# Kernel optimization log

Measured on AMD Instinct MI355X. Metric: run time of the kernel, lower is better.

## Reference

```python
import jax, jax.numpy as jnp
import numpy as np

B, S, D = 4, 1024, 4096
HQ, HKV, HD = 32, 8, 128
GROUPS = HQ // HKV
SCALE = 1.0 / np.sqrt(HD)


def setup_inputs() -> dict:
    key = jax.random.key(0)
    ks = jax.random.split(key, 7)
    inv_freq = 1.0 / (10000.0 ** (jnp.arange(0, HD, 2, dtype=jnp.float32) / HD))
    pos = jnp.arange(S, dtype=jnp.float32)
    freqs = pos[:, None] * inv_freq[None, :]           # [S, HD/2]
    emb = jnp.concatenate([freqs, freqs], axis=-1)      # [S, HD] (duplicated halves)
    return {
        "hidden_states": jax.random.normal(ks[0], (B, S, D), dtype=jnp.float32) * 0.02,
        "cos": jnp.cos(emb)[None],                       # [1, S, HD]
        "sin": jnp.sin(emb)[None],                       # [1, S, HD]
        "Wq": jax.random.normal(ks[1], (HQ * HD, D), dtype=jnp.float32) * 0.02,
        "Wk": jax.random.normal(ks[2], (HKV * HD, D), dtype=jnp.float32) * 0.02,
        "Wv": jax.random.normal(ks[3], (HKV * HD, D), dtype=jnp.float32) * 0.02,
        "Wo": jax.random.normal(ks[4], (D, HQ * HD), dtype=jnp.float32) * 0.02,
    }


def _rope(x, cos_h, sin_h):
    # x: [B, S, H, HD]; cos_h/sin_h: [S, HD/2] (non-interleaved rotate-half)
    half = x.shape[-1] // 2
    x1, x2 = x[..., :half], x[..., half:]
    c = cos_h[None, :, None, :]
    s = sin_h[None, :, None, :]
    return jnp.concatenate([x1 * c - x2 * s, x2 * c + x1 * s], axis=-1)


def reference(hidden_states, cos, sin, Wq, Wk, Wv, Wo):
    b, s, d = hidden_states.shape
    # projections (torch Linear: y = x @ W.T)
    q = (hidden_states @ Wq.T).reshape(b, s, HQ, HD)
    k = (hidden_states @ Wk.T).reshape(b, s, HKV, HD)
    v = (hidden_states @ Wv.T).reshape(b, s, HKV, HD)
    # module slices the second half of the [1, S, HD] tables
    cos_h = cos[0, :, HD // 2:]
    sin_h = sin[0, :, HD // 2:]
    q = _rope(q, cos_h, sin_h)
    k = _rope(k, cos_h, sin_h)
    # GQA: repeat each kv head GROUPS times (consecutively, as repeat_kv does)
    k = jnp.repeat(k, GROUPS, axis=2)                    # [B, S, HQ, HD]
    v = jnp.repeat(v, GROUPS, axis=2)
    # full (non-causal) SDPA, as in the source (no mask passed)
    scores = jnp.einsum("bqhd,bkhd->bhqk", q, k) * SCALE
    probs = jax.nn.softmax(scores, axis=-1)
    attn = jnp.einsum("bhqk,bkhd->bqhd", probs, v)
    attn = attn.reshape(b, s, HQ * HD)
    return attn @ Wo.T
```

## Files before the change

kernel.cpp:

```cpp
#include <hip/hip_runtime.h>
#include <hip/hip_bf16.h>
#include <stdint.h>


typedef __attribute__((ext_vector_type(8))) short s8_t;
typedef __attribute__((ext_vector_type(4))) float f4_t;
typedef __attribute__((ext_vector_type(4))) unsigned short us4_t;

#define MFMA16(a, b, c) __builtin_amdgcn_mfma_f32_16x16x32_bf16((a), (b), (c), 0, 0, 0)

__device__ __forceinline__ float b2f(unsigned short u) {
  union { unsigned int i; float f; } x; x.i = ((unsigned int)u) << 16; return x.f;
}
__device__ __forceinline__ unsigned short f2b(float f) {
  union { float f; unsigned int i; } x; x.f = f;
  unsigned int r = x.i + 0x7fff + ((x.i >> 16) & 1);
  return (unsigned short)(r >> 16);
}

__device__ __forceinline__ bool probe_is_f32_off(const void* p, int off) {
  if (!p) return false;
  const unsigned short* u = (const unsigned short*)p + off;
  bool f = false;
#pragma unroll
  for (int i = 0; i < 64; ++i) {
    const float v = b2f(u[i]);
    f |= !(fabsf(v) < 1e8f);
  }
  return f;
}
__device__ __forceinline__ bool probe_is_f32(const void* p) {
  return probe_is_f32_off(p, 0);
}

__device__ __forceinline__ s8_t cvt8(const float* p) {
  const float4 a = *(const float4*)(p);
  const float4 b = *(const float4*)(p + 4);
  union { s8_t v; __hip_bfloat162 h[4]; } t;
  t.h[0] = __float22bfloat162_rn(make_float2(a.x, a.y));
  t.h[1] = __float22bfloat162_rn(make_float2(a.z, a.w));
  t.h[2] = __float22bfloat162_rn(make_float2(b.x, b.y));
  t.h[3] = __float22bfloat162_rn(make_float2(b.z, b.w));
  return t.v;
}

__device__ __forceinline__ s8_t load8(const void* base, size_t off, bool f32) {
  if (f32) return cvt8((const float*)base + off);
  return *(const s8_t*)((const unsigned short*)base + off);
}

__global__ __launch_bounds__(256) void cvt_to_bf16(
    unsigned short* __restrict__ out, const void* __restrict__ in)
{
  const bool f = probe_is_f32(in);
  const size_t i = ((size_t)blockIdx.x * 256 + threadIdx.x) * 8;
  if (f) *(s8_t*)(out + i) = cvt8((const float*)in + i);
  else   *(s8_t*)(out + i) = *(const s8_t*)((const unsigned short*)in + i);
}

__global__ __launch_bounds__(256) void gemm_bt(
    void* __restrict__ C,
    const void* __restrict__ A,
    const void* __restrict__ B,
    int M, int N, int K,
    const void* probeA, const void* probeB, const void* probeC,
    int transC)
{
  constexpr int LP = 72;
  __shared__ unsigned short sA[128 * LP];
  __shared__ unsigned short sB[128 * LP];
  const bool fA = probe_is_f32(probeA);
  const bool fB = probe_is_f32(probeB);
  const bool fC = probe_is_f32(probeC);

  const int tid  = threadIdx.x;
  const int lane = tid & 63;
  const int wv   = tid >> 6;
  const int wr   = (wv >> 1) * 64;
  const int wc   = (wv & 1) * 64;
  const int quad = lane >> 4;
  const int l16  = lane & 15;
  const int m0 = blockIdx.x * 128;
  const int n0 = blockIdx.y * 128;

  f4_t acc[4][4];
#pragma unroll
  for (int i = 0; i < 4; ++i)
#pragma unroll
    for (int j = 0; j < 4; ++j) acc[i][j] = (f4_t){0.f, 0.f, 0.f, 0.f};

  int srow[4], scol[4];
#pragma unroll
  for (int it = 0; it < 4; ++it) {
    const int s = it * 256 + tid;
    srow[it] = s >> 3;
    scol[it] = (s & 7) * 8;
  }

  const int nK = K >> 6;
  for (int kt = 0; kt < nK; ++kt) {
    const int k0 = kt << 6;
    s8_t va[4], vb[4];
#pragma unroll
    for (int it = 0; it < 4; ++it) {
      va[it] = load8(A, (size_t)(m0 + srow[it]) * K + k0 + scol[it], fA);
      vb[it] = load8(B, (size_t)(n0 + srow[it]) * K + k0 + scol[it], fB);
    }
#pragma unroll
    for (int it = 0; it < 4; ++it) {
      *(s8_t*)(&sA[srow[it] * LP + scol[it]]) = va[it];
      *(s8_t*)(&sB[srow[it] * LP + scol[it]]) = vb[it];
    }
    __syncthreads();
#pragma unroll
    for (int kc = 0; kc < 2; ++kc) {
      s8_t af[4], bf[4];
#pragma unroll
      for (int i = 0; i < 4; ++i) {
        af[i] = *(const s8_t*)(&sA[(wr + i * 16 + l16) * LP + (kc * 4 + quad) * 8]);
        bf[i] = *(const s8_t*)(&sB[(wc + i * 16 + l16) * LP + (kc * 4 + quad) * 8]);
      }
#pragma unroll
      for (int i = 0; i < 4; ++i)
#pragma unroll
        for (int j = 0; j < 4; ++j)
          acc[i][j] = MFMA16(af[i], bf[j], acc[i][j]);
    }
    __syncthreads();
  }

  if (transC) {
#pragma unroll
    for (int i = 0; i < 4; ++i) {
      const int rbase = m0 + wr + i * 16 + quad * 4;
#pragma unroll
      for (int j = 0; j < 4; ++j) {
        const int col = n0 + wc + j * 16 + l16;
        us4_t t;
#pragma unroll
        for (int rg = 0; rg < 4; ++rg) t[rg] = f2b(acc[i][j][rg]);
        *(us4_t*)(&((unsigned short*)C)[(size_t)col * M + rbase]) = t;
      }
    }
  } else {
#pragma unroll
    for (int i = 0; i < 4; ++i) {
      const int rbase = m0 + wr + i * 16 + quad * 4;
#pragma unroll
      for (int j = 0; j < 4; ++j) {
        const int col = n0 + wc + j * 16 + l16;
#pragma unroll
        for (int rg = 0; rg < 4; ++rg) {
          const size_t idx = (size_t)(rbase + rg) * N + col;
          if (fC) ((float*)C)[idx] = acc[i][j][rg];
          else    ((unsigned short*)C)[idx] = f2b(acc[i][j][rg]);
        }
      }
    }
  }
}

__global__ __launch_bounds__(256) void rope_kernel(
    unsigned short* __restrict__ X,
    const void* __restrict__ cosb,
    const void* __restrict__ sinb,
    int log2nh, int mode)
{
  bool f;
  if (mode == 1)      f = true;
  else if (mode == 2) f = false;
  else f = probe_is_f32_off(cosb, 2048) | probe_is_f32_off(sinb, 2048);
  const size_t idx = (size_t)blockIdx.x * 256 + threadIdx.x;
  const int jb = (int)(idx & 7) * 8;
  const size_t row = idx >> 3;
  const int s = (int)((row >> log2nh) & 1023);
  unsigned short* p = X + row * 128;
  union { s8_t v; unsigned short u[8]; } ua, ub, o1, o2;
  ua.v = *(const s8_t*)(p + jb);
  ub.v = *(const s8_t*)(p + 64 + jb);
#pragma unroll
  for (int j = 0; j < 8; ++j) {
    const int ci = s * 128 + 64 + jb + j;
    const float c  = f ? ((const float*)cosb)[ci] : b2f(((const unsigned short*)cosb)[ci]);
    const float sn = f ? ((const float*)sinb)[ci] : b2f(((const unsigned short*)sinb)[ci]);
    const float x1 = b2f(ua.u[j]);
    const float x2 = b2f(ub.u[j]);
    o1.u[j] = f2b(x1 * c - x2 * sn);
    o2.u[j] = f2b(x2 * c + x1 * sn);
  }
  *(s8_t*)(p + jb)      = o1.v;
  *(s8_t*)(p + 64 + jb) = o2.v;
}

__global__ __launch_bounds__(256) void attn_kernel(
    unsigned short* O,
    const unsigned short* Q,
    const unsigned short* __restrict__ Kb,
    const unsigned short* __restrict__ Vt)
{
  constexpr int S = 1024, HQ = 32, HKV = 8, HD = 128;
  constexpr int SCP = 1048;
  constexpr int QP  = 152;
  constexpr float SCALE = 0.08838834764831845f;
  __shared__ unsigned short sc[16 * SCP];
  __shared__ unsigned short sq[16 * QP];
  __shared__ float s_linv[16];

  const int bid = blockIdx.x;
  const int qt = bid & 63;
  const int h  = (bid >> 6) & 31;
  const int b  = bid >> 11;
  const int kh = h >> 2;
  const int tid  = threadIdx.x;
  const int lane = tid & 63;
  const int wv   = tid >> 6;
  const int quad = lane >> 4;
  const int l16  = lane & 15;

  const unsigned short* Qg = Q  + ((size_t)(b * S + qt * 16) * HQ + h) * HD;
  const unsigned short* Kg = Kb + ((size_t)b * S * HKV + kh) * HD;
  const unsigned short* Vg = Vt + ((size_t)kh * HD) * 4096 + (size_t)b * S;

  {
    const int r = tid >> 4, c = (tid & 15) * 8;
    *(s8_t*)(&sq[r * QP + c]) = *(const s8_t*)(Qg + (size_t)r * (HQ * HD) + c);
  }
  __syncthreads();

#pragma unroll 2
  for (int kt = 0; kt < 16; ++kt) {
    const int ks = wv * 256 + kt * 16;
    f4_t acc = (f4_t){0.f, 0.f, 0.f, 0.f};
#pragma unroll
    for (int kc = 0; kc < 4; ++kc) {
      const s8_t qa = *(const s8_t*)(&sq[l16 * QP + kc * 32 + quad * 8]);
      const s8_t kf = *(const s8_t*)(Kg + (size_t)(ks + l16) * (HKV * HD) + kc * 32 + quad * 8);
      acc = MFMA16(qa, kf, acc);
    }
#pragma unroll
    for (int rg = 0; rg < 4; ++rg)
      sc[(quad * 4 + rg) * SCP + ks + l16] = f2b(acc[rg] * SCALE);
  }
  __syncthreads();

  {
    const int r = tid >> 4, c0 = tid & 15;
    unsigned short* srow = &sc[r * SCP + c0 * 8];
    float mx = -1e30f;
#pragma unroll
    for (int u = 0; u < 8; ++u) {
      union { s8_t v; unsigned short us[8]; } t;
      t.v = *(const s8_t*)(srow + u * 128);
#pragma unroll
      for (int j = 0; j < 8; ++j) mx = fmaxf(mx, b2f(t.us[j]));
    }
#pragma unroll
    for (int off = 8; off; off >>= 1) mx = fmaxf(mx, __shfl_xor(mx, off, 16));
    float sum = 0.f;
#pragma unroll
    for (int u = 0; u < 8; ++u) {
      union { s8_t v; unsigned short us[8]; } t;
      t.v = *(const s8_t*)(srow + u * 128);
#pragma unroll
      for (int j = 0; j < 8; ++j) {
        const float e = __expf(b2f(t.us[j]) - mx);
        sum += e;
        t.us[j] = f2b(e);
      }
      *(s8_t*)(srow + u * 128) = t.v;
    }
#pragma unroll
    for (int off = 8; off; off >>= 1) sum += __shfl_xor(sum, off, 16);
    if (c0 == 0) s_linv[r] = 1.0f / sum;
  }
  __syncthreads();

  f4_t oacc[2];
  oacc[0] = (f4_t){0.f, 0.f, 0.f, 0.f};
  oacc[1] = (f4_t){0.f, 0.f, 0.f, 0.f};
  const unsigned short* vb0 = Vg + (size_t)(wv * 32 + l16) * 4096 + quad * 8;
  const unsigned short* vb1 = vb0 + (size_t)16 * 4096;
  const unsigned short* prow = &sc[l16 * SCP + quad * 8];
#pragma unroll 2
  for (int ck = 0; ck < 16; ++ck) {
#pragma unroll
    for (int kc = 0; kc < 2; ++kc) {
      const int ko = ck * 64 + kc * 32;
      const s8_t pa = *(const s8_t*)(prow + ko);
      const s8_t v0 = *(const s8_t*)(vb0 + ko);
      const s8_t v1 = *(const s8_t*)(vb1 + ko);
      oacc[0] = MFMA16(pa, v0, oacc[0]);
      oacc[1] = MFMA16(pa, v1, oacc[1]);
    }
  }

#pragma unroll
  for (int dt = 0; dt < 2; ++dt)
#pragma unroll
    for (int rg = 0; rg < 4; ++rg) {
      const int r = quad * 4 + rg;
      const int d = wv * 32 + dt * 16 + l16;
      O[((size_t)(b * S + qt * 16 + r) * HQ + h) * HD + d] =
          f2b(oacc[dt][rg] * s_linv[r]);
    }
}

extern "C" void kernel_launch(void* const* d_in, const int* in_sizes, int n_in,
                              void* d_out, int out_size, void* d_ws, size_t ws_size,
                              hipStream_t stream)
{
  const void* hs   = d_in[0];
  const void* cosb = d_in[1];
  const void* sinb = d_in[2];
  const void* Wq   = d_in[3];
  const void* Wk   = d_in[4];
  const void* Wv   = d_in[5];
  const void* Wo   = d_in[6];

  const size_t MB = (size_t)1 << 20;
  const bool f32in = (n_in >= 1 && in_sizes && in_sizes[0] == (int)(64 * MB));
  int rmode = 0;
  if (in_sizes && n_in >= 2) {
    if (in_sizes[1] == 524288) rmode = 1;
    else if (in_sizes[1] == 262144) rmode = 2;
  }

  unsigned short* Qb = (unsigned short*)d_ws;
  unsigned short* Kb = (unsigned short*)d_out;
  unsigned short* Vt = (unsigned short*)d_out + 4194304;

  const void* hsA = hs;
  if (f32in && out_size >= (int)(48 * MB)) {
    unsigned short* hs_b = (unsigned short*)d_out + 8388608;
    cvt_to_bf16<<<8192, 256, 0, stream>>>(hs_b, hs);
    hsA = hs_b;
  }
  const void* WqB = Wq;
  if (f32in && ws_size >= 64 * MB) {
    unsigned short* wq_b = (unsigned short*)d_ws + 16777216;
    cvt_to_bf16<<<8192, 256, 0, stream>>>(wq_b, Wq);
    WqB = wq_b;
  }
  const void* WoB = Wo;
  if (f32in && ws_size >= 96 * MB) {
    unsigned short* wo_b = (unsigned short*)d_ws + 33554432;
    cvt_to_bf16<<<8192, 256, 0, stream>>>(wo_b, Wo);
    WoB = wo_b;
  }

  gemm_bt<<<dim3(32,  8), 256, 0, stream>>>(Kb, hsA, Wk, 4096, 1024, 4096,
                                            hsA, Wk, nullptr, 0);
  gemm_bt<<<dim3(32,  8), 256, 0, stream>>>(Vt, hsA, Wv, 4096, 1024, 4096,
                                            hsA, Wv, nullptr, 1);
  gemm_bt<<<dim3(32, 32), 256, 0, stream>>>(Qb, hsA, WqB, 4096, 4096, 4096,
                                            hsA, WqB, nullptr, 0);
  rope_kernel<<<4096, 256, 0, stream>>>(Qb, cosb, sinb, 5, rmode);
  rope_kernel<<<1024, 256, 0, stream>>>(Kb, cosb, sinb, 3, rmode);
  attn_kernel<<<4 * 32 * 64, 256, 0, stream>>>(Qb, Qb, Kb, Vt);
  gemm_bt<<<dim3(32, 32), 256, 0, stream>>>(d_out, Qb, WoB, 4096, 4096, 4096,
                                            nullptr, WoB, hs, 0);
}
```

Before: 1.939 ms.

## Use direct global-to-LDS loads in GEMM, pre-convert Wk/Wv, tune attention kernel

```diff
diff --git a/kernel.cpp b/kernel.cpp
--- a/kernel.cpp
+++ b/kernel.cpp
@@ -16,6 +16,13 @@
   union { float f; unsigned int i; } x; x.f = f;
   unsigned int r = x.i + 0x7fff + ((x.i >> 16) & 1);
   return (unsigned short)(r >> 16);
+}
+
+__device__ __forceinline__ void gload16(const unsigned short* g, unsigned short* l) {
+  __builtin_amdgcn_global_load_lds(
+      (const __attribute__((address_space(1))) void*)(uintptr_t)g,
+      (__attribute__((address_space(3))) void*)(unsigned int)(uintptr_t)l,
+      16, 0, 0);
 }
 
 __device__ __forceinline__ bool probe_is_f32_off(const void* p, int off) {
@@ -98,35 +105,66 @@
   }
 
   const int nK = K >> 6;
-  for (int kt = 0; kt < nK; ++kt) {
-    const int k0 = kt << 6;
-    s8_t va[4], vb[4];
-#pragma unroll
-    for (int it = 0; it < 4; ++it) {
-      va[it] = load8(A, (size_t)(m0 + srow[it]) * K + k0 + scol[it], fA);
-      vb[it] = load8(B, (size_t)(n0 + srow[it]) * K + k0 + scol[it], fB);
-    }
-#pragma unroll
-    for (int it = 0; it < 4; ++it) {
-      *(s8_t*)(&sA[srow[it] * LP + scol[it]]) = va[it];
-      *(s8_t*)(&sB[srow[it] * LP + scol[it]]) = vb[it];
-    }
-    __syncthreads();
-#pragma unroll
-    for (int kc = 0; kc < 2; ++kc) {
-      s8_t af[4], bf[4];
-#pragma unroll
-      for (int i = 0; i < 4; ++i) {
-        af[i] = *(const s8_t*)(&sA[(wr + i * 16 + l16) * LP + (kc * 4 + quad) * 8]);
-        bf[i] = *(const s8_t*)(&sB[(wc + i * 16 + l16) * LP + (kc * 4 + quad) * 8]);
-      }
-#pragma unroll
-      for (int i = 0; i < 4; ++i)
-#pragma unroll
-        for (int j = 0; j < 4; ++j)
-          acc[i][j] = MFMA16(af[i], bf[j], acc[i][j]);
-    }
-    __syncthreads();
+
+  if (!fA && !fB) {
+    const unsigned short* Ag = (const unsigned short*)A;
+    const unsigned short* Bg = (const unsigned short*)B;
+    for (int kt = 0; kt < nK; ++kt) {
+      const int k0 = kt << 6;
+#pragma unroll
+      for (int it = 0; it < 4; ++it) {
+        const int s = it * 256 + tid;
+        gload16(Ag + (size_t)(m0 + srow[it]) * K + k0 + scol[it], &sA[s * 8]);
+        gload16(Bg + (size_t)(n0 + srow[it]) * K + k0 + scol[it], &sB[s * 8]);
+      }
+      __syncthreads();
+#pragma unroll
+      for (int kc = 0; kc < 2; ++kc) {
+        s8_t af[4], bfr[4];
+#pragma unroll
+        for (int i = 0; i < 4; ++i) {
+          af[i]  = *(const s8_t*)(&sA[(wr + i * 16 + l16) * 64 + (kc * 4 + quad) * 8]);
+          bfr[i] = *(const s8_t*)(&sB[(wc + i * 16 + l16) * 64 + (kc * 4 + quad) * 8]);
+        }
+#pragma unroll
+        for (int i = 0; i < 4; ++i)
+#pragma unroll
+          for (int j = 0; j < 4; ++j)
+            acc[i][j] = MFMA16(af[i], bfr[j], acc[i][j]);
+      }
+      __syncthreads();
+    }
+  } else {
+    for (int kt = 0; kt < nK; ++kt) {
+      const int k0 = kt << 6;
+      s8_t va[4], vb[4];
+#pragma unroll
+      for (int it = 0; it < 4; ++it) {
+        va[it] = load8(A, (size_t)(m0 + srow[it]) * K + k0 + scol[it], fA);
+        vb[it] = load8(B, (size_t)(n0 + srow[it]) * K + k0 + scol[it], fB);
+      }
+#pragma unroll
+      for (int it = 0; it < 4; ++it) {
+        *(s8_t*)(&sA[srow[it] * LP + scol[it]]) = va[it];
+        *(s8_t*)(&sB[srow[it] * LP + scol[it]]) = vb[it];
+      }
+      __syncthreads();
+#pragma unroll
+      for (int kc = 0; kc < 2; ++kc) {
+        s8_t af[4], bfr[4];
+#pragma unroll
+        for (int i = 0; i < 4; ++i) {
+          af[i]  = *(const s8_t*)(&sA[(wr + i * 16 + l16) * LP + (kc * 4 + quad) * 8]);
+          bfr[i] = *(const s8_t*)(&sB[(wc + i * 16 + l16) * LP + (kc * 4 + quad) * 8]);
+        }
+#pragma unroll
+        for (int i = 0; i < 4; ++i)
+#pragma unroll
+          for (int j = 0; j < 4; ++j)
+            acc[i][j] = MFMA16(af[i], bfr[j], acc[i][j]);
+      }
+      __syncthreads();
+    }
   }
 
   if (transC) {
@@ -192,7 +230,7 @@
   *(s8_t*)(p + 64 + jb) = o2.v;
 }
 
-__global__ __launch_bounds__(256) void attn_kernel(
+__global__ __launch_bounds__(256, 4) void attn_kernel(
     unsigned short* O,
     const unsigned short* Q,
     const unsigned short* __restrict__ Kb,
@@ -206,7 +244,7 @@
   __shared__ unsigned short sq[16 * QP];
   __shared__ float s_linv[16];
 
-  const int bid = blockIdx.x;
+  const int bid = (((int)blockIdx.x & 7) << 10) | ((int)blockIdx.x >> 3);
   const int qt = bid & 63;
   const int h  = (bid >> 6) & 31;
   const int b  = bid >> 11;
@@ -227,15 +265,18 @@
   }
   __syncthreads();
 
+  s8_t qa[4];
+#pragma unroll
+  for (int kc = 0; kc < 4; ++kc)
+    qa[kc] = *(const s8_t*)(&sq[l16 * QP + kc * 32 + quad * 8]);
 #pragma unroll 2
   for (int kt = 0; kt < 16; ++kt) {
     const int ks = wv * 256 + kt * 16;
     f4_t acc = (f4_t){0.f, 0.f, 0.f, 0.f};
 #pragma unroll
     for (int kc = 0; kc < 4; ++kc) {
-      const s8_t qa = *(const s8_t*)(&sq[l16 * QP + kc * 32 + quad * 8]);
       const s8_t kf = *(const s8_t*)(Kg + (size_t)(ks + l16) * (HKV * HD) + kc * 32 + quad * 8);
-      acc = MFMA16(qa, kf, acc);
+      acc = MFMA16(qa[kc], kf, acc);
     }
 #pragma unroll
     for (int rg = 0; rg < 4; ++rg)
@@ -281,7 +322,7 @@
   const unsigned short* vb0 = Vg + (size_t)(wv * 32 + l16) * 4096 + quad * 8;
   const unsigned short* vb1 = vb0 + (size_t)16 * 4096;
   const unsigned short* prow = &sc[l16 * SCP + quad * 8];
-#pragma unroll 2
+#pragma unroll 4
   for (int ck = 0; ck < 16; ++ck) {
 #pragma unroll
     for (int kc = 0; kc < 2; ++kc) {
@@ -335,6 +376,16 @@
     cvt_to_bf16<<<8192, 256, 0, stream>>>(hs_b, hs);
     hsA = hs_b;
   }
+  const void* WkB = Wk;
+  const void* WvB = Wv;
+  if (f32in && out_size >= (int)(64 * MB)) {
+    unsigned short* wk_b = (unsigned short*)d_out + 25165824;
+    unsigned short* wv_b = (unsigned short*)d_out + 29360128;
+    cvt_to_bf16<<<2048, 256, 0, stream>>>(wk_b, Wk);
+    cvt_to_bf16<<<2048, 256, 0, stream>>>(wv_b, Wv);
+    WkB = wk_b;
+    WvB = wv_b;
+  }
   const void* WqB = Wq;
   if (f32in && ws_size >= 64 * MB) {
     unsigned short* wq_b = (unsigned short*)d_ws + 16777216;
@@ -348,10 +399,10 @@
     WoB = wo_b;
   }
 
-  gemm_bt<<<dim3(32,  8), 256, 0, stream>>>(Kb, hsA, Wk, 4096, 1024, 4096,
-                                            hsA, Wk, nullptr, 0);
-  gemm_bt<<<dim3(32,  8), 256, 0, stream>>>(Vt, hsA, Wv, 4096, 1024, 4096,
-                                            hsA, Wv, nullptr, 1);
+  gemm_bt<<<dim3(32,  8), 256, 0, stream>>>(Kb, hsA, WkB, 4096, 1024, 4096,
+                                            hsA, WkB, nullptr, 0);
+  gemm_bt<<<dim3(32,  8), 256, 0, stream>>>(Vt, hsA, WvB, 4096, 1024, 4096,
+                                            hsA, WvB, nullptr, 1);
   gemm_bt<<<dim3(32, 32), 256, 0, stream>>>(Qb, hsA, WqB, 4096, 4096, 4096,
                                             hsA, WqB, nullptr, 0);
   rope_kernel<<<4096, 256, 0, stream>>>(Qb, cosb, sinb, 5, rmode);
```

Measured after the change: 1.953 ms. No clear change (+0.7%).
